# Kernel optimization log

Measured on AMD Instinct MI355X. Metric: run time of the kernel, lower is better.

## Reference

```python
import jax, jax.numpy as jnp
import numpy as np

INPUT_DIM = 246
HIDDEN = 512
OUTPUT_DIM = 123
B, T = 128, 500
N_DIFF, N_ABIL = 11, 8


def setup_inputs() -> dict:
    key = jax.random.key(0)
    ks = jax.random.split(key, 9)
    feats = jax.random.normal(ks[0], (B, T, INPUT_DIM), dtype=jnp.float32)
    ability = jax.random.randint(ks[1], (B, T, 1), 0, N_ABIL).astype(jnp.float32)
    diff = jax.random.randint(ks[2], (B, T, 1), 0, N_DIFF).astype(jnp.float32)
    x = jnp.concatenate([feats, ability, diff], axis=-1)  # [B,T,248]
    in_dim = INPUT_DIM + N_DIFF + N_ABIL  # 265
    s_ih = 1.0 / np.sqrt(HIDDEN)
    W_ih = jax.random.uniform(ks[3], (4 * HIDDEN, in_dim), jnp.float32, -s_ih, s_ih)
    W_hh = jax.random.uniform(ks[4], (4 * HIDDEN, HIDDEN), jnp.float32, -s_ih, s_ih)
    b_ih = jax.random.uniform(ks[5], (4 * HIDDEN,), jnp.float32, -s_ih, s_ih)
    b_hh = jax.random.uniform(ks[6], (4 * HIDDEN,), jnp.float32, -s_ih, s_ih)
    s_fc = 1.0 / np.sqrt(HIDDEN)
    W_fc = jax.random.uniform(ks[7], (OUTPUT_DIM, HIDDEN), jnp.float32, -s_fc, s_fc)
    b_fc = jax.random.uniform(ks[8], (OUTPUT_DIM,), jnp.float32, -s_fc, s_fc)
    return {"x": x, "W_ih": W_ih, "W_hh": W_hh, "b_ih": b_ih, "b_hh": b_hh,
            "W_fc": W_fc, "b_fc": b_fc}


def _lstm(x, W_ih, W_hh, b_ih, b_hh):
    # x: [B,T,In] -> out: [B,T,H]; PyTorch gate order i,f,g,o
    Bsz = x.shape[0]
    H = W_hh.shape[1]
    x_proj = jnp.einsum('bti,gi->btg', x, W_ih) + b_ih + b_hh  # [B,T,4H]

    def step(carry, xt):
        h, c = carry
        gates = xt + h @ W_hh.T
        i, f, g, o = jnp.split(gates, 4, axis=-1)
        i, f, o = jax.nn.sigmoid(i), jax.nn.sigmoid(f), jax.nn.sigmoid(o)
        g = jnp.tanh(g)
        c = f * c + i * g
        h = o * jnp.tanh(c)
        return (h, c), h

    h0 = jnp.zeros((Bsz, H), x.dtype)
    c0 = jnp.zeros((Bsz, H), x.dtype)
    (_, _), hs = jax.lax.scan(step, (h0, c0), x_proj.transpose(1, 0, 2))
    return hs.transpose(1, 0, 2)


def reference(x, W_ih, W_hh, b_ih, b_hh, W_fc, b_fc):
    feats = x[..., :INPUT_DIM]
    ability = x[..., -2].astype(jnp.int32)
    diff = x[..., -1].astype(jnp.int32)
    one_hot_diff = jax.nn.one_hot(diff, N_DIFF, dtype=x.dtype)
    one_hot_ab = jax.nn.one_hot(ability, N_ABIL, dtype=x.dtype)
    new_x = jnp.tanh(jnp.concatenate([feats, one_hot_diff, one_hot_ab], axis=-1))
    out = _lstm(new_x, W_ih, W_hh, b_ih, b_hh)  # [B,T,H]
    res = jax.nn.sigmoid(jnp.einsum('bth,oh->bto', out, W_fc) + b_fc)
    return res[:, :-1, :]
```

## Files before the change

kernel.cpp:

```cpp
#include <hip/hip_runtime.h>
#include <hip/hip_fp16.h>


typedef _Float16 f16;
typedef _Float16 f16x8 __attribute__((ext_vector_type(8)));
typedef float f32x4 __attribute__((ext_vector_type(4)));
typedef unsigned u32x4 __attribute__((ext_vector_type(4)));

#define TS 499

#define NEWX_OFF   0ul
#define NEWX_BYTES (500ul*8*10240)
#define HALL_OFF   (NEWX_OFF + NEWX_BYTES)
#define HALL_BYTES (500ul*128*512*2)
#define WHH_OFF    (HALL_OFF + HALL_BYTES)
#define WHH_BYTES  (2048ul*512*2)
#define WIH_OFF    (WHH_OFF + WHH_BYTES)
#define WIH_BYTES  (2048ul*288*2)
#define WFC_OFF    (WIH_OFF + WIH_BYTES)
#define WFC_BYTES  (128ul*512*2)
#define BIAS_OFF   (WFC_OFF + WFC_BYTES)
#define BIAS_BYTES (2048ul*4)
#define CNT_OFF    (BIAS_OFF + BIAS_BYTES)
#define CNT_BYTES  (4096ul)
#define WS_NEED    (CNT_OFF + CNT_BYTES)

__device__ __forceinline__ float tanh_dev(float x) {
    float ax = fabsf(x);
    float e  = __expf(-2.f * ax);
    float r  = (1.f - e) / (1.f + e);
    return copysignf(r, x);
}
__device__ __forceinline__ float sigm_dev(float x) {
    float e = __expf(-fabsf(x));
    float p = 1.f / (1.f + e);
    return x >= 0.f ? p : 1.f - p;
}

__device__ __forceinline__ void llc_store_nowait(unsigned* p, unsigned v) {
    asm volatile("global_store_dword %0, %1, off sc0 sc1" :: "v"(p), "v"(v) : "memory");
}
__device__ __forceinline__ unsigned llc_load_u32(const unsigned* p) {
    unsigned v;
    asm volatile("global_load_dword %0, %1, off sc0 sc1\n\ts_waitcnt vmcnt(0)"
                 : "=v"(v) : "v"(p) : "memory");
    return v;
}

__global__ void __launch_bounds__(256) prep_newx(const float* __restrict__ x,
                                                 f16* __restrict__ newx) {
    const int t  = blockIdx.x;
    const int bt = blockIdx.y;
    const int tid = threadIdx.x;
    char* tb = (char*)newx + ((size_t)t * 8 + bt) * 10240;
    for (int idx = tid; idx < 16 * 288; idx += 256) {
        const int r = idx / 288, k = idx - r * 288;
        const float* xr = x + ((size_t)(bt * 16 + r) * 500 + t) * 248;
        float v;
        if (k < 246)      v = tanh_dev(xr[k]);
        else if (k < 257) v = (k - 246 == (int)xr[247]) ? 0.76159415595576485f : 0.f;
        else if (k < 265) v = (k - 257 == (int)xr[246]) ? 0.76159415595576485f : 0.f;
        else              v = 0.f;
        const int byte = r * 640 + ((((k >> 3) ^ (r & 7)) << 4) | ((k & 7) << 1));
        *(f16*)(tb + byte) = (f16)v;
    }
}

__global__ void __launch_bounds__(256) prep_w(const float* __restrict__ W_ih,
                                              const float* __restrict__ W_hh,
                                              const float* __restrict__ W_fc,
                                              const float* __restrict__ b_ih,
                                              const float* __restrict__ b_hh,
                                              f16* __restrict__ whh, f16* __restrict__ wih,
                                              f16* __restrict__ wfc, float* __restrict__ bias) {
    const int NHH = 2048 * 512;
    const int NIH = 2048 * 288;
    const int NFC = 128 * 512;
    const int NT  = NHH + NIH + NFC + 2048;
    for (int i = blockIdx.x * 256 + threadIdx.x; i < NT; i += gridDim.x * 256) {
        if (i < NHH) {
            whh[i] = (f16)W_hh[i];
        } else if (i < NHH + NIH) {
            int j2 = i - NHH; int rr = j2 / 288, kk = j2 % 288;
            wih[j2] = (kk < 265) ? (f16)W_ih[rr * 265 + kk] : (f16)0.f;
        } else if (i < NHH + NIH + NFC) {
            int j2 = i - (NHH + NIH); int rr = j2 >> 9, kk = j2 & 511;
            wfc[j2] = (rr < 123) ? (f16)W_fc[rr * 512 + kk] : (f16)0.f;
        } else {
            int j2 = i - (NHH + NIH + NFC);
            bias[j2] = b_ih[j2] + b_hh[j2];
        }
    }
}

__global__ void __launch_bounds__(512, 1) lstm_seq(const f16* __restrict__ newx_,
                                                   f16* __restrict__ hall,
                                                   const f16* __restrict__ whh,
                                                   const f16* __restrict__ wih,
                                                   const float* __restrict__ bias,
                                                   unsigned* __restrict__ cnt) {
    __shared__ __align__(16) char hsb[16 * 1024];
    __shared__ __align__(16) char xsb[16 * 640];
    __shared__ float gf[4 * 16 * 32];
    __shared__ __align__(16) f16 hout[512];

    const char* newx = (const char*)newx_;
    const int tid = threadIdx.x, bid = blockIdx.x;
    const int btile = bid & 7;
    const int hsl   = bid >> 3;

    const int w = tid >> 6, wl = tid & 63;
    const int arow = wl & 15, kgrp = wl >> 4;
    const int g = w & 3, cb = w >> 2;
    const int grow = g * 512 + hsl * 32 + cb * 16 + arow;
    const int bE = tid >> 5, colE = tid & 31;

    f16x8 wh[16], wi[9];
    #pragma unroll
    for (int kc = 0; kc < 16; ++kc)
        wh[kc] = *(const f16x8*)(whh + (size_t)grow * 512 + kc * 32 + kgrp * 8);
    #pragma unroll
    for (int kc = 0; kc < 9; ++kc)
        wi[kc] = *(const f16x8*)(wih + (size_t)grow * 288 + kc * 32 + kgrp * 8);
    const float bb = bias[grow];

    unsigned* const flags  = cnt + 512 + btile * 32;
    unsigned* const myflag = flags + hsl;

    const int row1 = tid >> 6, c16w = tid & 63;
    const int hw1 = row1 * 1024 + ((c16w ^ (row1 & 7)) << 4);
    const int hw2 = (row1 + 8) * 1024 + ((c16w ^ (row1 & 7)) << 4);
    const int swq = arow & 7;

    float c_st = 0.f;

    u32x4 xra, xrb;
    {
        const char* xt = newx + (size_t)btile * 10240;
        xra = *(const u32x4*)(xt + tid * 16);
        if (tid < 128) xrb = *(const u32x4*)(xt + 8192 + tid * 16);
    }

    for (int t = 0; t < TS; ++t) {
        if (t > 0) {
            int spins = 0;
            for (;;) {
                unsigned f = (unsigned)t;
                if (wl < 16) f = llc_load_u32(flags + wl);
                if (__ballot(f >= (unsigned)t) == ~0ull) break;
                __builtin_amdgcn_s_sleep(2);
                if (++spins > (1 << 15)) break;
            }
            const char* hp0 = (const char*)(hall + ((size_t)(t - 1) * 128 + btile * 16) * 512)
                              + tid * 16;
            const char* hp1 = hp0 + 8192;
            u32x4 h0, h1;
            asm volatile("global_load_dwordx4 %0, %2, off sc0 sc1\n\t"
                         "global_load_dwordx4 %1, %3, off sc0 sc1\n\t"
                         "s_waitcnt vmcnt(0)"
                         : "=&v"(h0), "=&v"(h1) : "v"(hp0), "v"(hp1) : "memory");
            *(u32x4*)(hsb + hw1) = h0;
            *(u32x4*)(hsb + hw2) = h1;
        }
        *(u32x4*)(xsb + tid * 16) = xra;
        if (tid < 128) *(u32x4*)(xsb + 8192 + tid * 16) = xrb;
        __syncthreads();

        f32x4 acc = {bb, bb, bb, bb};
        #pragma unroll
        for (int kc = 0; kc < 9; ++kc) {
            f16x8 a = *(const f16x8*)(xsb + arow * 640 + (((kc * 4 + kgrp) ^ swq) << 4));
            acc = __builtin_amdgcn_mfma_f32_16x16x32_f16(a, wi[kc], acc, 0, 0, 0);
        }
        if (t > 0) {
            f32x4 e0 = {0.f, 0.f, 0.f, 0.f}, e1 = {0.f, 0.f, 0.f, 0.f};
            #pragma unroll
            for (int kc = 0; kc < 16; kc += 2) {
                f16x8 a0 = *(const f16x8*)(hsb + arow * 1024 + (((kc * 4 + kgrp) ^ swq) << 4));
                f16x8 a1 = *(const f16x8*)(hsb + arow * 1024 + ((((kc + 1) * 4 + kgrp) ^ swq) << 4));
                e0 = __builtin_amdgcn_mfma_f32_16x16x32_f16(a0, wh[kc],     e0, 0, 0, 0);
                e1 = __builtin_amdgcn_mfma_f32_16x16x32_f16(a1, wh[kc + 1], e1, 0, 0, 0);
            }
            acc += e0; acc += e1;
        }

        {
            const char* xt1 = newx + ((size_t)(t + 1) * 8 + btile) * 10240;
            xra = *(const u32x4*)(xt1 + tid * 16);
            if (tid < 128) xrb = *(const u32x4*)(xt1 + 8192 + tid * 16);
        }

        {
            float* gp = gf + g * 512 + cb * 16 + (wl & 15);
            const int b4 = (wl >> 4) * 4;
            gp[(b4 + 0) * 32] = acc[0];
            gp[(b4 + 1) * 32] = acc[1];
            gp[(b4 + 2) * 32] = acc[2];
            gp[(b4 + 3) * 32] = acc[3];
        }
        __syncthreads();

        {
            const float* gq = gf + bE * 32 + colE;
            float iv = sigm_dev(gq[0]);
            float fv = sigm_dev(gq[512]);
            float gv = tanh_dev(gq[1024]);
            float ov = sigm_dev(gq[1536]);
            c_st = fv * c_st + iv * gv;
            float hv = ov * tanh_dev(c_st);
            hout[bE * 32 + colE] = (f16)hv;
        }
        __syncthreads();

        if (tid < 64) {
            u32x4 hv4 = *(const u32x4*)((const char*)hout + tid * 16);
            const f16* sp = hall + ((size_t)t * 128 + btile * 16 + (tid >> 2)) * 512
                            + hsl * 32 + (tid & 3) * 8;
            asm volatile("global_store_dwordx4 %0, %1, off sc0 sc1\n\t"
                         "s_waitcnt vmcnt(0)"
                         :: "v"(sp), "v"(hv4) : "memory");
            if (tid == 0) llc_store_nowait(myflag, (unsigned)(t + 1));
        }
    }
}

__global__ void __launch_bounds__(256) out_gemm(const f16* __restrict__ hall,
                                                const f16* __restrict__ wfc,
                                                const float* __restrict__ bfc,
                                                float* __restrict__ out) {
    const int tid = threadIdx.x;
    const int w = tid >> 6, wl = tid & 63;
    const int arow = wl & 15, kgrp = wl >> 4;
    const long m0 = (long)blockIdx.x * 64 + w * 16;
    const f16* ap = hall + (m0 + arow) * 512 + kgrp * 8;
    f16x8 a[16];
    #pragma unroll
    for (int kc = 0; kc < 16; ++kc) a[kc] = *(const f16x8*)(ap + kc * 32);
    #pragma unroll
    for (int jt = 0; jt < 8; ++jt) {
        f32x4 acc = {0.f, 0.f, 0.f, 0.f};
        const f16* bp = wfc + (size_t)(jt * 16 + arow) * 512 + kgrp * 8;
        #pragma unroll
        for (int kc = 0; kc < 16; ++kc)
            acc = __builtin_amdgcn_mfma_f32_16x16x32_f16(a[kc], *(const f16x8*)(bp + kc * 32),
                                                         acc, 0, 0, 0);
        const int col = jt * 16 + arow;
        if (col < 123) {
            const float bv = bfc[col];
            #pragma unroll
            for (int rr = 0; rr < 4; ++rr) {
                long m = m0 + kgrp * 4 + rr;
                int tt = (int)(m >> 7), b = (int)(m & 127);
                out[((size_t)b * 499 + tt) * 123 + col] = sigm_dev(acc[rr] + bv);
            }
        }
    }
}

extern "C" void kernel_launch(void* const* d_in, const int* in_sizes, int n_in,
                              void* d_out, int out_size, void* d_ws, size_t ws_size,
                              hipStream_t stream) {
    if (ws_size < WS_NEED) return;

    const float* x    = (const float*)d_in[0];
    const float* W_ih = (const float*)d_in[1];
    const float* W_hh = (const float*)d_in[2];
    const float* b_ih = (const float*)d_in[3];
    const float* b_hh = (const float*)d_in[4];
    const float* W_fc = (const float*)d_in[5];
    const float* b_fc = (const float*)d_in[6];
    float* out = (float*)d_out;
    char* ws = (char*)d_ws;

    f16* newx   = (f16*)(ws + NEWX_OFF);
    f16* hall   = (f16*)(ws + HALL_OFF);
    f16* whh    = (f16*)(ws + WHH_OFF);
    f16* wih    = (f16*)(ws + WIH_OFF);
    f16* wfc    = (f16*)(ws + WFC_OFF);
    float* bias = (float*)(ws + BIAS_OFF);
    unsigned* cnt = (unsigned*)(ws + CNT_OFF);

    (void)hipMemsetAsync(cnt, 0, CNT_BYTES, stream);

    prep_newx<<<dim3(TS, 8), 256, 0, stream>>>(x, newx);
    prep_w<<<512, 256, 0, stream>>>(W_ih, W_hh, W_fc, b_ih, b_hh, whh, wih, wfc, bias);

    void* args[6] = {&newx, &hall, &whh, &wih, &bias, &cnt};
    (void)hipLaunchCooperativeKernel((const void*)lstm_seq, dim3(128), dim3(512), args,
                                     0, stream);

    out_gemm<<<998, 256, 0, stream>>>(hall, wfc, b_fc, out);
}
```

Measured before the change: 1.541 ms.

## Restructure LSTM step: register-resident x operands, early input GEMM, single-wave flag polling

The precomputed input tile is re-laid out so each lane loads its MFMA A-fragments for x directly into registers, removing the x shared-memory staging and its barrier. The input projection now runs before waiting on the other blocks, which hides some of the inter-block wait. Only wave 0 polls the global flags and then releases the other waves through a shared-memory token. Flags are padded to separate cache lines, the gate buffer gets a padded stride to reduce bank conflicts, and the wave that stores h rotates every step. The cost is more registers and a spin-wait on shared memory.

```diff
diff --git a/kernel.cpp b/kernel.cpp
--- a/kernel.cpp
+++ b/kernel.cpp
@@ -10,7 +10,7 @@
 #define TS 499
 
 #define NEWX_OFF   0ul
-#define NEWX_BYTES (500ul*8*10240)
+#define NEWX_BYTES (500ul*8*9216)
 #define HALL_OFF   (NEWX_OFF + NEWX_BYTES)
 #define HALL_BYTES (500ul*128*512*2)
 #define WHH_OFF    (HALL_OFF + HALL_BYTES)
@@ -22,7 +22,7 @@
 #define BIAS_OFF   (WFC_OFF + WFC_BYTES)
 #define BIAS_BYTES (2048ul*4)
 #define CNT_OFF    (BIAS_OFF + BIAS_BYTES)
-#define CNT_BYTES  (4096ul)
+#define CNT_BYTES  (8192ul)
 #define WS_NEED    (CNT_OFF + CNT_BYTES)
 
 __device__ __forceinline__ float tanh_dev(float x) {
@@ -52,7 +52,7 @@
     const int t  = blockIdx.x;
     const int bt = blockIdx.y;
     const int tid = threadIdx.x;
-    char* tb = (char*)newx + ((size_t)t * 8 + bt) * 10240;
+    char* tb = (char*)newx + ((size_t)t * 8 + bt) * 9216;
     for (int idx = tid; idx < 16 * 288; idx += 256) {
         const int r = idx / 288, k = idx - r * 288;
         const float* xr = x + ((size_t)(bt * 16 + r) * 500 + t) * 248;
@@ -61,7 +61,8 @@
         else if (k < 257) v = (k - 246 == (int)xr[247]) ? 0.76159415595576485f : 0.f;
         else if (k < 265) v = (k - 257 == (int)xr[246]) ? 0.76159415595576485f : 0.f;
         else              v = 0.f;
-        const int byte = r * 640 + ((((k >> 3) ^ (r & 7)) << 4) | ((k & 7) << 1));
+        const int col8 = k >> 3;
+        const int byte = (col8 >> 2) * 1024 + (((col8 & 3) * 16 + r) << 4) + ((k & 7) << 1);
         *(f16*)(tb + byte) = (f16)v;
     }
 }
@@ -100,9 +101,9 @@
                                                    const float* __restrict__ bias,
                                                    unsigned* __restrict__ cnt) {
     __shared__ __align__(16) char hsb[16 * 1024];
-    __shared__ __align__(16) char xsb[16 * 640];
-    __shared__ float gf[4 * 16 * 32];
+    __shared__ float gf[4 * 560];
     __shared__ __align__(16) f16 hout[512];
+    __shared__ volatile int tok;
 
     const char* newx = (const char*)newx_;
     const int tid = threadIdx.x, bid = blockIdx.x;
@@ -124,60 +125,75 @@
         wi[kc] = *(const f16x8*)(wih + (size_t)grow * 288 + kc * 32 + kgrp * 8);
     const float bb = bias[grow];
 
-    unsigned* const flags  = cnt + 512 + btile * 32;
-    unsigned* const myflag = flags + hsl;
-
-    const int row1 = tid >> 6, c16w = tid & 63;
-    const int hw1 = row1 * 1024 + ((c16w ^ (row1 & 7)) << 4);
-    const int hw2 = (row1 + 8) * 1024 + ((c16w ^ (row1 & 7)) << 4);
-    const int swq = arow & 7;
+    unsigned* const flags  = cnt + btile * 256;
+    unsigned* const myflag = flags + hsl * 16;
+
+    const int srow = tid & 15, sc8 = tid >> 4;
+    const int soff1 = (sc8 >> 2) * 1024 + (((sc8 & 3) * 16 + srow) << 4);
+    const int soff2 = soff1 + 8 * 1024;
 
     float c_st = 0.f;
 
-    u32x4 xra, xrb;
+    f16x8 xa[9];
     {
-        const char* xt = newx + (size_t)btile * 10240;
-        xra = *(const u32x4*)(xt + tid * 16);
-        if (tid < 128) xrb = *(const u32x4*)(xt + 8192 + tid * 16);
-    }
+        const char* xt = newx + (size_t)btile * 9216;
+        #pragma unroll
+        for (int kc = 0; kc < 9; ++kc)
+            xa[kc] = *(const f16x8*)(xt + kc * 1024 + wl * 16);
+    }
+
+    if (tid == 0) tok = 0;
+    __syncthreads();
 
     for (int t = 0; t < TS; ++t) {
-        if (t > 0) {
-            int spins = 0;
-            for (;;) {
-                unsigned f = (unsigned)t;
-                if (wl < 16) f = llc_load_u32(flags + wl);
-                if (__ballot(f >= (unsigned)t) == ~0ull) break;
-                __builtin_amdgcn_s_sleep(2);
-                if (++spins > (1 << 15)) break;
-            }
-            const char* hp0 = (const char*)(hall + ((size_t)(t - 1) * 128 + btile * 16) * 512)
-                              + tid * 16;
-            const char* hp1 = hp0 + 8192;
-            u32x4 h0, h1;
-            asm volatile("global_load_dwordx4 %0, %2, off sc0 sc1\n\t"
-                         "global_load_dwordx4 %1, %3, off sc0 sc1\n\t"
-                         "s_waitcnt vmcnt(0)"
-                         : "=&v"(h0), "=&v"(h1) : "v"(hp0), "v"(hp1) : "memory");
-            *(u32x4*)(hsb + hw1) = h0;
-            *(u32x4*)(hsb + hw2) = h1;
-        }
-        *(u32x4*)(xsb + tid * 16) = xra;
-        if (tid < 128) *(u32x4*)(xsb + 8192 + tid * 16) = xrb;
-        __syncthreads();
-
         f32x4 acc = {bb, bb, bb, bb};
         #pragma unroll
-        for (int kc = 0; kc < 9; ++kc) {
-            f16x8 a = *(const f16x8*)(xsb + arow * 640 + (((kc * 4 + kgrp) ^ swq) << 4));
-            acc = __builtin_amdgcn_mfma_f32_16x16x32_f16(a, wi[kc], acc, 0, 0, 0);
-        }
+        for (int kc = 0; kc < 9; ++kc)
+            acc = __builtin_amdgcn_mfma_f32_16x16x32_f16(xa[kc], wi[kc], acc, 0, 0, 0);
+        {
+            const char* xt1 = newx + ((size_t)(t + 1) * 8 + btile) * 9216;
+            #pragma unroll
+            for (int kc = 0; kc < 9; ++kc)
+                xa[kc] = *(const f16x8*)(xt1 + kc * 1024 + wl * 16);
+        }
+
         if (t > 0) {
-            f32x4 e0 = {0.f, 0.f, 0.f, 0.f}, e1 = {0.f, 0.f, 0.f, 0.f};
+            if (tid < 64) {
+                int spins = 0;
+                for (;;) {
+                    unsigned f = (unsigned)t;
+                    if (wl < 16) f = llc_load_u32(flags + wl * 16);
+                    if (__ballot(f >= (unsigned)t) == ~0ull) break;
+                    __builtin_amdgcn_s_sleep(1);
+                    if (++spins > (1 << 15)) break;
+                }
+                if (tid == 0) tok = t;
+            } else {
+                int spins = 0;
+                while (tok < t) {
+                    __builtin_amdgcn_s_sleep(1);
+                    if (++spins > (1 << 17)) break;
+                }
+            }
+            {
+                const char* hb = (const char*)hall + ((size_t)(t - 1) * 128 + btile * 16) * 1024;
+                const char* ga1 = hb + srow * 1024 + sc8 * 16;
+                const char* ga2 = ga1 + 512;
+                u32x4 h0, h1;
+                asm volatile("global_load_dwordx4 %0, %2, off sc0 sc1\n\t"
+                             "global_load_dwordx4 %1, %3, off sc0 sc1\n\t"
+                             "s_waitcnt vmcnt(0)"
+                             : "=&v"(h0), "=&v"(h1) : "v"(ga1), "v"(ga2) : "memory");
+                *(u32x4*)(hsb + soff1) = h0;
+                *(u32x4*)(hsb + soff2) = h1;
+            }
+            __syncthreads();
+
+            f32x4 e0 = {0.f,0.f,0.f,0.f}, e1 = {0.f,0.f,0.f,0.f};
             #pragma unroll
             for (int kc = 0; kc < 16; kc += 2) {
-                f16x8 a0 = *(const f16x8*)(hsb + arow * 1024 + (((kc * 4 + kgrp) ^ swq) << 4));
-                f16x8 a1 = *(const f16x8*)(hsb + arow * 1024 + ((((kc + 1) * 4 + kgrp) ^ swq) << 4));
+                f16x8 a0 = *(const f16x8*)(hsb + kc * 1024 + wl * 16);
+                f16x8 a1 = *(const f16x8*)(hsb + (kc + 1) * 1024 + wl * 16);
                 e0 = __builtin_amdgcn_mfma_f32_16x16x32_f16(a0, wh[kc],     e0, 0, 0, 0);
                 e1 = __builtin_amdgcn_mfma_f32_16x16x32_f16(a1, wh[kc + 1], e1, 0, 0, 0);
             }
@@ -185,41 +201,35 @@
         }
 
         {
-            const char* xt1 = newx + ((size_t)(t + 1) * 8 + btile) * 10240;
-            xra = *(const u32x4*)(xt1 + tid * 16);
-            if (tid < 128) xrb = *(const u32x4*)(xt1 + 8192 + tid * 16);
-        }
+            float* gp = gf + g * 560 + cb * 16 + (wl & 15);
+            const int b4 = (wl >> 4) * 4;
+            gp[(b4 + 0) * 35] = acc[0];
+            gp[(b4 + 1) * 35] = acc[1];
+            gp[(b4 + 2) * 35] = acc[2];
+            gp[(b4 + 3) * 35] = acc[3];
+        }
+        __syncthreads();
 
         {
-            float* gp = gf + g * 512 + cb * 16 + (wl & 15);
-            const int b4 = (wl >> 4) * 4;
-            gp[(b4 + 0) * 32] = acc[0];
-            gp[(b4 + 1) * 32] = acc[1];
-            gp[(b4 + 2) * 32] = acc[2];
-            gp[(b4 + 3) * 32] = acc[3];
-        }
-        __syncthreads();
-
-        {
-            const float* gq = gf + bE * 32 + colE;
+            const float* gq = gf + bE * 35 + colE;
             float iv = sigm_dev(gq[0]);
-            float fv = sigm_dev(gq[512]);
-            float gv = tanh_dev(gq[1024]);
-            float ov = sigm_dev(gq[1536]);
+            float fv = sigm_dev(gq[560]);
+            float gv = tanh_dev(gq[1120]);
+            float ov = sigm_dev(gq[1680]);
             c_st = fv * c_st + iv * gv;
             float hv = ov * tanh_dev(c_st);
             hout[bE * 32 + colE] = (f16)hv;
         }
         __syncthreads();
 
-        if (tid < 64) {
-            u32x4 hv4 = *(const u32x4*)((const char*)hout + tid * 16);
-            const f16* sp = hall + ((size_t)t * 128 + btile * 16 + (tid >> 2)) * 512
-                            + hsl * 32 + (tid & 3) * 8;
+        if ((tid >> 6) == (t & 7)) {
+            u32x4 hv4 = *(const u32x4*)((const char*)hout + wl * 16);
+            const f16* sp = hall + ((size_t)t * 128 + btile * 16 + (wl >> 2)) * 512
+                            + hsl * 32 + (wl & 3) * 8;
             asm volatile("global_store_dwordx4 %0, %1, off sc0 sc1\n\t"
                          "s_waitcnt vmcnt(0)"
                          :: "v"(sp), "v"(hv4) : "memory");
-            if (tid == 0) llc_store_nowait(myflag, (unsigned)(t + 1));
+            if (wl == 0) llc_store_nowait(myflag, (unsigned)(t + 1));
         }
     }
 }
```

New measurement: 1.486 ms. -3.6%, faster.
